# Performance work log

Hardware: AMD Instinct MI355X
Metric: run time of the kernel (lower is better)

Reference implementation:

```python
import jax, jax.numpy as jnp
import numpy as np

# DCT-III (a.k.a. IDCT), unnormalized, scaled to match the DREAMPlace kernel:
#   y_k = x_0 + 2 * sum_{n=1}^{N-1} x_n * cos(pi * n * (2k+1) / (2N))
# (the docstring's Re{1/2 x0 + sum xn e^{j pi n (2k+1)/(2N)}} scaled by 2).
# Computed in O(N log N) via a length-2N FFT:
#   y_k = Re{ sum_n c_n x_n e^{j pi n/(2N)} e^{2 pi j n k/(2N)} }
# which is 2N * ifft(pad(a, 2N)) evaluated at k = 0..N-1, with
#   a_n = c_n * x_n * exp(j pi n / (2N)),  c_0 = 1, c_{n>0} = 2.

def _idct_last_dim(x):
    N = x.shape[-1]
    n = jnp.arange(N)
    c = jnp.where(n == 0, 1.0, 2.0).astype(x.dtype)
    twiddle = jnp.exp(1j * (jnp.pi / (2 * N)) * n.astype(jnp.float32)).astype(jnp.complex64)
    a = (c * x).astype(jnp.complex64) * twiddle          # [.., N]
    y = jnp.fft.ifft(a, n=2 * N, axis=-1)                # [.., 2N]
    return (y.real[..., :N] * (2 * N)).astype(x.dtype)


def setup_inputs() -> dict:
    key = jax.random.key(0)
    x = jax.random.normal(key, (4096, 4096), dtype=jnp.float32)
    return {"x": x}


def reference(x) -> jnp.ndarray:
    return _idct_last_dim(x)
```

## Files before the change

kernel.cpp:

```cpp
#include <hip/hip_runtime.h>
#include <cstdint>


#define NN 4096
#define HH 2048
#define BM 128
#define BN 128
#define BK 128
#define NT (HH / BK)

typedef int i32x4 __attribute__((ext_vector_type(4)));
typedef int i32x2 __attribute__((ext_vector_type(2)));

__device__ __forceinline__ void async_copy16(void* lds_base, const void* gptr) {
    __builtin_amdgcn_global_load_lds(
        (const __attribute__((address_space(1))) unsigned int*)gptr,
        (__attribute__((address_space(3))) unsigned int*)lds_base,
        16, 0, 0);
}

__device__ __forceinline__ int pack4(int q0, int q1, int q2, int q3) {
    return (q0 & 255) | ((q1 & 255) << 8) | ((q2 & 255) << 16) | ((q3 & 255) << 24);
}

__global__ __launch_bounds__(256) void prep_i8(const float* __restrict__ x,
                                               signed char* __restrict__ Ae,
                                               signed char* __restrict__ Ao,
                                               signed char* __restrict__ CEm,
                                               signed char* __restrict__ COm,
                                               float* __restrict__ se,
                                               float* __restrict__ so) {
    const int b = blockIdx.x;
    const int t = threadIdx.x;
    const float s = 3.834951969714103e-4f;

    if (b < 4096) {
        __shared__ float wmaxe[4], wmaxo[4];
        const float* xr = x + (size_t)b * NN;
        float v[16];
#pragma unroll
        for (int j = 0; j < 4; ++j) {
            float4 f = ((const float4*)xr)[t * 4 + j];
            v[j * 4 + 0] = f.x; v[j * 4 + 1] = f.y;
            v[j * 4 + 2] = f.z; v[j * 4 + 3] = f.w;
        }
        float emax = 1e-30f, omax = 1e-30f;
#pragma unroll
        for (int i = 0; i < 8; ++i) {
            emax = fmaxf(emax, __builtin_fabsf(v[2 * i]));
            omax = fmaxf(omax, __builtin_fabsf(v[2 * i + 1]));
        }
#pragma unroll
        for (int m = 1; m < 64; m <<= 1) {
            emax = fmaxf(emax, __shfl_xor(emax, m));
            omax = fmaxf(omax, __shfl_xor(omax, m));
        }
        const int wv = t >> 6;
        if ((t & 63) == 0) { wmaxe[wv] = emax; wmaxo[wv] = omax; }
        __syncthreads();
        const float rmax_e = fmaxf(fmaxf(wmaxe[0], wmaxe[1]), fmaxf(wmaxe[2], wmaxe[3]));
        const float rmax_o = fmaxf(fmaxf(wmaxo[0], wmaxo[1]), fmaxf(wmaxo[2], wmaxo[3]));
        const float inv_e = 127.0f / rmax_e, inv_o = 127.0f / rmax_o;
        int qe[8], qo[8];
#pragma unroll
        for (int i = 0; i < 8; ++i) {
            qe[i] = (int)rintf(v[2 * i] * inv_e);
            qo[i] = (int)rintf(v[2 * i + 1] * inv_o);
        }
        i32x2 oe, oo;
        oe[0] = pack4(qe[0], qe[1], qe[2], qe[3]);
        oe[1] = pack4(qe[4], qe[5], qe[6], qe[7]);
        oo[0] = pack4(qo[0], qo[1], qo[2], qo[3]);
        oo[1] = pack4(qo[4], qo[5], qo[6], qo[7]);
        ((i32x2*)(Ae + (size_t)b * HH))[t] = oe;
        ((i32x2*)(Ao + (size_t)b * HH))[t] = oo;
        if (t == 0) {
            se[b] = rmax_e * (1.0f / 127.0f);
            so[b] = rmax_o * (1.0f / 127.0f);
        }
    } else if (b < 6144) {
        const int k = b - 4096;
        const int twok1 = 2 * k + 1;
        int q[8];
#pragma unroll
        for (int i = 0; i < 8; ++i) {
            int m = t * 8 + i;
            int p = (2 * m * twok1) & 16383;
            float w = (m == 0) ? 1.0f : 2.0f;
            q[i] = (int)rintf(w * __cosf((float)p * s) * 63.5f);
        }
        i32x2 o;
        o[0] = pack4(q[0], q[1], q[2], q[3]);
        o[1] = pack4(q[4], q[5], q[6], q[7]);
        ((i32x2*)(CEm + (size_t)k * HH))[t] = o;
    } else {
        const int k = b - 6144;
        const int twok1 = 2 * k + 1;
        int q[8];
#pragma unroll
        for (int i = 0; i < 8; ++i) {
            int m = t * 8 + i;
            int p = ((2 * m + 1) * twok1) & 16383;
            q[i] = (int)rintf(__cosf((float)p * s) * 127.0f);
        }
        i32x2 o;
        o[0] = pack4(q[0], q[1], q[2], q[3]);
        o[1] = pack4(q[4], q[5], q[6], q[7]);
        ((i32x2*)(COm + (size_t)k * HH))[t] = o;
    }
}

__global__ __launch_bounds__(512, 2) void idct_gemm2(const signed char* __restrict__ Ae,
                                                     const signed char* __restrict__ Ao,
                                                     const signed char* __restrict__ CEm,
                                                     const signed char* __restrict__ COm,
                                                     const float* __restrict__ se,
                                                     const float* __restrict__ so,
                                                     float* __restrict__ C) {
    __shared__ __align__(16) signed char sAe[2][BM * BK];
    __shared__ __align__(16) signed char sAo[2][BM * BK];
    __shared__ __align__(16) signed char sCE[2][BN * BK];
    __shared__ __align__(16) signed char sCO[2][BN * BK];

    const int tid  = threadIdx.x;
    const int wave = tid >> 6;
    const int lane = tid & 63;
    const int waveM = wave >> 2;
    const int waveN = wave & 3;

    const int rowBase = blockIdx.y * BM;
    const int colBase = blockIdx.x * BN;

    i32x4 accE[4][2] = {};
    i32x4 accO[4][2] = {};

    const int srow  = lane >> 3;
    const int sgran = lane & 7;
    const int ggcol = (sgran ^ srow) * 16;
    const int rmod  = lane & 7;
    const int quad  = lane >> 4;
    const int ck0   = wave * 2;

    const size_t aRow = (size_t)(rowBase + ck0 * 8 + srow) * HH + ggcol;
    const size_t bRow = (size_t)(colBase + ck0 * 8 + srow) * HH + ggcol;

#define STAGE(BUF, K0)                                                        \
    do {                                                                      \
        _Pragma("unroll")                                                     \
        for (int j = 0; j < 2; ++j) {                                         \
            size_t aoff = aRow + (size_t)j * 8 * HH + (size_t)(K0);           \
            size_t boff = bRow + (size_t)j * 8 * HH + (size_t)(K0);           \
            async_copy16(&sAe[BUF][(ck0 + j) * 1024], Ae + aoff);             \
            async_copy16(&sAo[BUF][(ck0 + j) * 1024], Ao + aoff);             \
            async_copy16(&sCE[BUF][(ck0 + j) * 1024], CEm + boff);            \
            async_copy16(&sCO[BUF][(ck0 + j) * 1024], COm + boff);            \
        }                                                                     \
    } while (0)

#define COMPUTE(BUF)                                                          \
    do {                                                                      \
        _Pragma("unroll")                                                     \
        for (int kk = 0; kk < 2; ++kk) {                                      \
            const int poff = ((kk * 4 + quad) ^ rmod) * 16;                   \
            i32x4 af[4], bfr[2];                                              \
            _Pragma("unroll")                                                 \
            for (int mi = 0; mi < 4; ++mi)                                    \
                af[mi] = *(const i32x4*)&sAe[BUF][(waveM * 64 + mi * 16 + (lane & 15)) * BK + poff]; \
            _Pragma("unroll")                                                 \
            for (int ni = 0; ni < 2; ++ni)                                    \
                bfr[ni] = *(const i32x4*)&sCE[BUF][(waveN * 32 + ni * 16 + (lane & 15)) * BK + poff]; \
            __builtin_amdgcn_s_setprio(1);                                    \
            _Pragma("unroll")                                                 \
            for (int mi = 0; mi < 4; ++mi)                                    \
                _Pragma("unroll")                                             \
                for (int ni = 0; ni < 2; ++ni)                                \
                    accE[mi][ni] = __builtin_amdgcn_mfma_i32_16x16x64_i8(     \
                        af[mi], bfr[ni], accE[mi][ni], 0, 0, 0);              \
            __builtin_amdgcn_s_setprio(0);                                    \
            _Pragma("unroll")                                                 \
            for (int mi = 0; mi < 4; ++mi)                                    \
                af[mi] = *(const i32x4*)&sAo[BUF][(waveM * 64 + mi * 16 + (lane & 15)) * BK + poff]; \
            _Pragma("unroll")                                                 \
            for (int ni = 0; ni < 2; ++ni)                                    \
                bfr[ni] = *(const i32x4*)&sCO[BUF][(waveN * 32 + ni * 16 + (lane & 15)) * BK + poff]; \
            __builtin_amdgcn_s_setprio(1);                                    \
            _Pragma("unroll")                                                 \
            for (int mi = 0; mi < 4; ++mi)                                    \
                _Pragma("unroll")                                             \
                for (int ni = 0; ni < 2; ++ni)                                \
                    accO[mi][ni] = __builtin_amdgcn_mfma_i32_16x16x64_i8(     \
                        af[mi], bfr[ni], accO[mi][ni], 0, 0, 0);              \
            __builtin_amdgcn_s_setprio(0);                                    \
        }                                                                     \
    } while (0)

    STAGE(0, 0);
    asm volatile("s_waitcnt vmcnt(0)" ::: "memory");
    __builtin_amdgcn_s_barrier();

#pragma unroll 1
    for (int t = 0; t < NT; t += 2) {
        STAGE(1, (t + 1) * BK);
        COMPUTE(0);
        asm volatile("s_waitcnt vmcnt(0) lgkmcnt(0)" ::: "memory");
        __builtin_amdgcn_s_barrier();

        if (t + 2 < NT) STAGE(0, (t + 2) * BK);
        COMPUTE(1);
        asm volatile("s_waitcnt vmcnt(0) lgkmcnt(0)" ::: "memory");
        __builtin_amdgcn_s_barrier();
    }
#undef STAGE
#undef COMPUTE

    const float sB_s = 2.0f / 127.0f;
    const int mrow0 = rowBase + waveM * 64 + (lane >> 4) * 4;
    const int ncol0 = colBase + waveN * 32 + (lane & 15);
#pragma unroll
    for (int mi = 0; mi < 4; ++mi)
#pragma unroll
        for (int ni = 0; ni < 2; ++ni)
#pragma unroll
            for (int rg = 0; rg < 4; ++rg) {
                int rr = mrow0 + mi * 16 + rg;
                int cc = ncol0 + ni * 16;
                float e = (float)accE[mi][ni][rg] * (se[rr] * sB_s);
                float o = (float)accO[mi][ni][rg] * (so[rr] * sB_s);
                C[(size_t)rr * NN + cc] = e + o;
                C[(size_t)rr * NN + (NN - 1 - cc)] = e - o;
            }
}

__global__ __launch_bounds__(256) void idct_naive(const float* __restrict__ x,
                                                  float* __restrict__ out) {
    int row = blockIdx.x;
    __shared__ float sx[NN];
    for (int i = threadIdx.x; i < NN; i += 256) sx[i] = x[(size_t)row * NN + i];
    __syncthreads();
    const float s = 3.834951969714103e-4f;
    for (int k = threadIdx.x; k < NN; k += 256) {
        int twok1 = 2 * k + 1;
        float acc = sx[0];
        int p = 0;
        for (int n = 1; n < NN; ++n) {
            p += twok1; p &= 16383;
            acc += 2.0f * sx[n] * __cosf((float)p * s);
        }
        out[(size_t)row * NN + k] = acc;
    }
}

extern "C" void kernel_launch(void* const* d_in, const int* in_sizes, int n_in,
                              void* d_out, int out_size, void* d_ws, size_t ws_size,
                              hipStream_t stream) {
    const float* x = (const float*)d_in[0];
    float* out = (float*)d_out;

    const size_t eA = (size_t)NN * HH;
    const size_t eC = (size_t)HH * HH;
    const size_t need = 2 * eA + 2 * eC + 2 * NN * sizeof(float);

    if (ws_size >= need) {
        signed char* Ae = (signed char*)d_ws;
        signed char* Ao = Ae + eA;
        signed char* CEm = Ao + eA;
        signed char* COm = CEm + eC;
        float* se = (float*)(COm + eC);
        float* so = se + NN;

        prep_i8<<<8192, 256, 0, stream>>>(x, Ae, Ao, CEm, COm, se, so);

        dim3 grid(HH / BN, NN / BM);
        idct_gemm2<<<grid, 512, 0, stream>>>(Ae, Ao, CEm, COm, se, so, out);
    } else {
        idct_naive<<<NN, 256, 0, stream>>>(x, out);
    }
}
```

Baseline: 160.0 us.

## Deepen int8 GEMM pipeline to four 64-wide K stages with interleaved loads

```diff
diff --git a/kernel.cpp b/kernel.cpp
--- a/kernel.cpp
+++ b/kernel.cpp
@@ -6,7 +6,7 @@
 #define HH 2048
 #define BM 128
 #define BN 128
-#define BK 128
+#define BK 64
 #define NT (HH / BK)
 
 typedef int i32x4 __attribute__((ext_vector_type(4)));
@@ -117,10 +117,10 @@
                                                      const float* __restrict__ se,
                                                      const float* __restrict__ so,
                                                      float* __restrict__ C) {
-    __shared__ __align__(16) signed char sAe[2][BM * BK];
-    __shared__ __align__(16) signed char sAo[2][BM * BK];
-    __shared__ __align__(16) signed char sCE[2][BN * BK];
-    __shared__ __align__(16) signed char sCO[2][BN * BK];
+    __shared__ __align__(16) signed char sAe[4][BM * BK];
+    __shared__ __align__(16) signed char sAo[4][BM * BK];
+    __shared__ __align__(16) signed char sCE[4][BN * BK];
+    __shared__ __align__(16) signed char sCO[4][BN * BK];
 
     const int tid  = threadIdx.x;
     const int wave = tid >> 6;
@@ -134,84 +134,74 @@
     i32x4 accE[4][2] = {};
     i32x4 accO[4][2] = {};
 
-    const int srow  = lane >> 3;
-    const int sgran = lane & 7;
-    const int ggcol = (sgran ^ srow) * 16;
-    const int rmod  = lane & 7;
+    const int srow  = lane >> 2;
+    const int sgran = lane & 3;
+    const int ggcol = (sgran ^ ((srow >> 1) & 3)) * 16;
     const int quad  = lane >> 4;
-    const int ck0   = wave * 2;
-
-    const size_t aRow = (size_t)(rowBase + ck0 * 8 + srow) * HH + ggcol;
-    const size_t bRow = (size_t)(colBase + ck0 * 8 + srow) * HH + ggcol;
-
-#define STAGE(BUF, K0)                                                        \
+    const int fsw   = (lane >> 1) & 3;
+    const int poff  = (quad ^ fsw) * 16;
+
+    const size_t aRow = (size_t)(rowBase + wave * 16 + srow) * HH + ggcol;
+    const size_t bRow = (size_t)(colBase + wave * 16 + srow) * HH + ggcol;
+
+#define PHASE(SA, SC, ACC, GA, GC, BUF, T, DOISSUE)                           \
     do {                                                                      \
+        i32x4 af[4], bfr[2];                                                  \
         _Pragma("unroll")                                                     \
-        for (int j = 0; j < 2; ++j) {                                         \
-            size_t aoff = aRow + (size_t)j * 8 * HH + (size_t)(K0);           \
-            size_t boff = bRow + (size_t)j * 8 * HH + (size_t)(K0);           \
-            async_copy16(&sAe[BUF][(ck0 + j) * 1024], Ae + aoff);             \
-            async_copy16(&sAo[BUF][(ck0 + j) * 1024], Ao + aoff);             \
-            async_copy16(&sCE[BUF][(ck0 + j) * 1024], CEm + boff);            \
-            async_copy16(&sCO[BUF][(ck0 + j) * 1024], COm + boff);            \
+        for (int mi = 0; mi < 4; ++mi)                                        \
+            af[mi] = *(const i32x4*)&SA[BUF][(waveM * 64 + mi * 16 + (lane & 15)) * BK + poff]; \
+        _Pragma("unroll")                                                     \
+        for (int ni = 0; ni < 2; ++ni)                                        \
+            bfr[ni] = *(const i32x4*)&SC[BUF][(waveN * 32 + ni * 16 + (lane & 15)) * BK + poff]; \
+        if (DOISSUE) {                                                        \
+            async_copy16(&SA[(BUF + 2) & 3][wave * 1024], GA + aRow + (size_t)((T) + 2) * BK); \
+            async_copy16(&SC[(BUF + 2) & 3][wave * 1024], GC + bRow + (size_t)((T) + 2) * BK); \
         }                                                                     \
-    } while (0)
-
-#define COMPUTE(BUF)                                                          \
-    do {                                                                      \
+        __builtin_amdgcn_s_barrier();                                         \
+        asm volatile("s_waitcnt lgkmcnt(0)" ::: "memory");                    \
+        __builtin_amdgcn_s_setprio(1);                                        \
         _Pragma("unroll")                                                     \
-        for (int kk = 0; kk < 2; ++kk) {                                      \
-            const int poff = ((kk * 4 + quad) ^ rmod) * 16;                   \
-            i32x4 af[4], bfr[2];                                              \
-            _Pragma("unroll")                                                 \
-            for (int mi = 0; mi < 4; ++mi)                                    \
-                af[mi] = *(const i32x4*)&sAe[BUF][(waveM * 64 + mi * 16 + (lane & 15)) * BK + poff]; \
+        for (int mi = 0; mi < 4; ++mi)                                        \
             _Pragma("unroll")                                                 \
             for (int ni = 0; ni < 2; ++ni)                                    \
-                bfr[ni] = *(const i32x4*)&sCE[BUF][(waveN * 32 + ni * 16 + (lane & 15)) * BK + poff]; \
-            __builtin_amdgcn_s_setprio(1);                                    \
-            _Pragma("unroll")                                                 \
-            for (int mi = 0; mi < 4; ++mi)                                    \
-                _Pragma("unroll")                                             \
-                for (int ni = 0; ni < 2; ++ni)                                \
-                    accE[mi][ni] = __builtin_amdgcn_mfma_i32_16x16x64_i8(     \
-                        af[mi], bfr[ni], accE[mi][ni], 0, 0, 0);              \
-            __builtin_amdgcn_s_setprio(0);                                    \
-            _Pragma("unroll")                                                 \
-            for (int mi = 0; mi < 4; ++mi)                                    \
-                af[mi] = *(const i32x4*)&sAo[BUF][(waveM * 64 + mi * 16 + (lane & 15)) * BK + poff]; \
-            _Pragma("unroll")                                                 \
-            for (int ni = 0; ni < 2; ++ni)                                    \
-                bfr[ni] = *(const i32x4*)&sCO[BUF][(waveN * 32 + ni * 16 + (lane & 15)) * BK + poff]; \
-            __builtin_amdgcn_s_setprio(1);                                    \
-            _Pragma("unroll")                                                 \
-            for (int mi = 0; mi < 4; ++mi)                                    \
-                _Pragma("unroll")                                             \
-                for (int ni = 0; ni < 2; ++ni)                                \
-                    accO[mi][ni] = __builtin_amdgcn_mfma_i32_16x16x64_i8(     \
-                        af[mi], bfr[ni], accO[mi][ni], 0, 0, 0);              \
-            __builtin_amdgcn_s_setprio(0);                                    \
-        }                                                                     \
+                ACC[mi][ni] = __builtin_amdgcn_mfma_i32_16x16x64_i8(          \
+                    af[mi], bfr[ni], ACC[mi][ni], 0, 0, 0);                   \
+        __builtin_amdgcn_s_setprio(0);                                        \
     } while (0)
 
-    STAGE(0, 0);
-    asm volatile("s_waitcnt vmcnt(0)" ::: "memory");
+#define STEP(BUF, T, DOISSUE, WAITN)                                          \
+    do {                                                                      \
+        PHASE(sAe, sCE, accE, Ae, CEm, BUF, T, DOISSUE);                      \
+        __builtin_amdgcn_s_barrier();                                         \
+        PHASE(sAo, sCO, accO, Ao, COm, BUF, T, DOISSUE);                      \
+        asm volatile("s_waitcnt vmcnt(" #WAITN ")" ::: "memory");             \
+        __builtin_amdgcn_s_barrier();                                         \
+    } while (0)
+
+    async_copy16(&sAe[0][wave * 1024], Ae + aRow);
+    async_copy16(&sAo[0][wave * 1024], Ao + aRow);
+    async_copy16(&sCE[0][wave * 1024], CEm + bRow);
+    async_copy16(&sCO[0][wave * 1024], COm + bRow);
+    async_copy16(&sAe[1][wave * 1024], Ae + aRow + BK);
+    async_copy16(&sAo[1][wave * 1024], Ao + aRow + BK);
+    async_copy16(&sCE[1][wave * 1024], CEm + bRow + BK);
+    async_copy16(&sCO[1][wave * 1024], COm + bRow + BK);
+    asm volatile("s_waitcnt vmcnt(4)" ::: "memory");
     __builtin_amdgcn_s_barrier();
 
 #pragma unroll 1
-    for (int t = 0; t < NT; t += 2) {
-        STAGE(1, (t + 1) * BK);
-        COMPUTE(0);
-        asm volatile("s_waitcnt vmcnt(0) lgkmcnt(0)" ::: "memory");
-        __builtin_amdgcn_s_barrier();
-
-        if (t + 2 < NT) STAGE(0, (t + 2) * BK);
-        COMPUTE(1);
-        asm volatile("s_waitcnt vmcnt(0) lgkmcnt(0)" ::: "memory");
-        __builtin_amdgcn_s_barrier();
-    }
-#undef STAGE
-#undef COMPUTE
+    for (int tb = 0; tb < 28; tb += 4) {
+        STEP(0, tb + 0, 1, 4);
+        STEP(1, tb + 1, 1, 4);
+        STEP(2, tb + 2, 1, 4);
+        STEP(3, tb + 3, 1, 4);
+    }
+    STEP(0, 28, 1, 4);
+    STEP(1, 29, 1, 4);
+    STEP(2, 30, 0, 0);
+    STEP(3, 31, 0, 0);
+#undef STEP
+#undef PHASE
 
     const float sB_s = 2.0f / 127.0f;
     const int mrow0 = rowBase + waveM * 64 + (lane >> 4) * 4;
```

Result: slower. 170.1 us (+6.3%).
